# Kernel optimization log

Measured on AMD Instinct MI355X. Metric: run time of the kernel, lower is better.

## Reference

```python
import jax, jax.numpy as jnp
import numpy as np

KK = 9  # 3x3 kernel taps
BN_EPS = 1e-5


def setup_inputs() -> dict:
    key = jax.random.key(0)
    ks = jax.random.split(key, 8)
    B, C, H, W = 2, 64, 256, 256
    O = 64
    x = jax.random.normal(ks[0], (B, C, H, W), dtype=jnp.float32)
    # offset/mask conv: 3*KK output channels (dy[9], dx[9], mask[9])
    w_off = jax.random.normal(ks[1], (3 * KK, C, 3, 3), dtype=jnp.float32) * 0.05
    b_off = jnp.zeros((3 * KK,), dtype=jnp.float32)
    # deformable conv weight
    w = jax.random.normal(ks[2], (O, C, 3, 3), dtype=jnp.float32) * (1.0 / np.sqrt(C * KK))
    b = jnp.zeros((O,), dtype=jnp.float32)
    gamma = jnp.ones((O,), dtype=jnp.float32)
    beta = jnp.zeros((O,), dtype=jnp.float32)
    return {"x": x, "w_off": w_off, "b_off": b_off, "w": w, "b": b,
            "gamma": gamma, "beta": beta}


def _dcn_bn_act_res(x, w_off, b_off, w, b, gamma, beta):
    B, C, H, W = x.shape
    O = w.shape[0]
    # offset/mask prediction via plain 3x3 conv
    om = jax.lax.conv_general_dilated(
        x, w_off, window_strides=(1, 1), padding=[(1, 1), (1, 1)],
        dimension_numbers=("NCHW", "OIHW", "NCHW")) + b_off[None, :, None, None]
    off_y = om[:, :KK]            # [B,9,H,W]
    off_x = om[:, KK:2 * KK]      # [B,9,H,W]
    mask = jax.nn.sigmoid(om[:, 2 * KK:])  # [B,9,H,W] modulation

    # absolute sampling coordinates: base grid + kernel tap offset (-1..1) + learned offset
    ky, kx = jnp.meshgrid(jnp.arange(3), jnp.arange(3), indexing="ij")
    ky = ky.reshape(KK).astype(jnp.float32) - 1.0
    kx = kx.reshape(KK).astype(jnp.float32) - 1.0
    hs = jnp.arange(H, dtype=jnp.float32)
    ws = jnp.arange(W, dtype=jnp.float32)
    py = off_y + hs[None, None, :, None] + ky[None, :, None, None]  # [B,9,H,W]
    px = off_x + ws[None, None, None, :] + kx[None, :, None, None]

    y0 = jnp.floor(py)
    x0 = jnp.floor(px)
    wy = py - y0
    wx = px - x0
    y0i = y0.astype(jnp.int32)
    x0i = x0.astype(jnp.int32)

    def gather(img, yi, xi):
        # img [C,H,W], yi/xi [9,H,W]; zero outside (implicit zero padding)
        valid = (yi >= 0) & (yi < H) & (xi >= 0) & (xi < W)
        yc = jnp.clip(yi, 0, H - 1)
        xc = jnp.clip(xi, 0, W - 1)
        return img[:, yc, xc] * valid[None].astype(img.dtype)  # [C,9,H,W]

    def sample_one(img, yi, xi, wy_, wx_):
        v00 = gather(img, yi, xi)
        v01 = gather(img, yi, xi + 1)
        v10 = gather(img, yi + 1, xi)
        v11 = gather(img, yi + 1, xi + 1)
        w00 = ((1 - wy_) * (1 - wx_))[None]
        w01 = ((1 - wy_) * wx_)[None]
        w10 = (wy_ * (1 - wx_))[None]
        w11 = (wy_ * wx_)[None]
        return v00 * w00 + v01 * w01 + v10 * w10 + v11 * w11  # [C,9,H,W]

    sampled = jax.vmap(sample_one)(x, y0i, x0i, wy, wx)  # [B,C,9,H,W]
    sampled = sampled * mask[:, None]

    out = jnp.einsum("bckhw,ock->bohw", sampled, w.reshape(O, C, KK))
    out = out + b[None, :, None, None]

    # BatchNorm (training-mode batch statistics)
    mu = out.mean(axis=(0, 2, 3), keepdims=True)
    var = out.var(axis=(0, 2, 3), keepdims=True)
    out = (out - mu) * jax.lax.rsqrt(var + BN_EPS)
    out = out * gamma[None, :, None, None] + beta[None, :, None, None]

    return jax.nn.relu(out) + x  # residual


def reference(x, w_off, b_off, w, b, gamma, beta):
    return _dcn_bn_act_res(x, w_off, b_off, w, b, gamma, beta)
```

## Files before the change

kernel.cpp:

```cpp
#include <hip/hip_runtime.h>
#include <hip/hip_fp16.h>
#include <math.h>

#define HWSZ 65536
#define IMGH 256
#define IMGW 256

typedef _Float16 half8 __attribute__((ext_vector_type(8)));
typedef float f32x4 __attribute__((ext_vector_type(4)));

__device__ inline unsigned short f2bf(float f) {
    unsigned u = __float_as_uint(f);
    return (unsigned short)((u + 0x7fffu + ((u >> 16) & 1u)) >> 16);
}
__device__ inline unsigned short f2h(float f) {
    __half h = __float2half(f);
    return __half_as_ushort(h);
}
__device__ inline __half2 duph2(unsigned s) {
    union { unsigned u; __half2 h; } c;
    c.u = (s & 0xffffu) * 0x10001u;
    return c.h;
}
__device__ inline void hacc(const uint4& q, __half2 w, __half2* v) {
    const __half2* h = (const __half2*)&q;
    v[0] = __hfma2(h[0], w, v[0]);
    v[1] = __hfma2(h[1], w, v[1]);
    v[2] = __hfma2(h[2], w, v[2]);
    v[3] = __hfma2(h[3], w, v[3]);
}

__global__ void prep_weights(const float* __restrict__ w_off,
                             const float* __restrict__ w,
                             unsigned short* __restrict__ wApack,
                             unsigned short* __restrict__ wOffPack) {
    int i = blockIdx.x * 256 + threadIdx.x;
    if (i < 36864) {
        int e = i;
        int j = e & 7, lane = (e >> 3) & 63, kk = (e >> 9) & 1;
        int t2 = e >> 10;
        int tap = t2 % 9, g = t2 / 9;
        int o = g * 16 + (lane & 15);
        int c = kk * 32 + ((lane >> 4) & 3) * 8 + j;
        wApack[e] = f2h(w[(o * 64 + c) * 9 + tap]);
    } else if (i < 36864 + 18432) {
        int e = i - 36864;
        int j = e & 7, lane = (e >> 3) & 63, kk = (e >> 9) & 1;
        int t2 = e >> 10;
        int tap = t2 % 9, mt = t2 / 9;
        int d = mt * 16 + (lane & 15);
        int c = kk * 32 + ((lane >> 4) & 3) * 8 + j;
        float v = (d < 27) ? w_off[(d * 64 + c) * 9 + tap] : 0.f;
        wOffPack[e] = f2h(v);
    }
}

__global__ __launch_bounds__(256) void transpose_x(const float* __restrict__ x,
                                                   unsigned short* __restrict__ xT) {
    __shared__ float tile[64 * 65];
    int blk = blockIdx.x;
    int b = blk >> 10;
    int p0 = (blk & 1023) * 64;
    int t = threadIdx.x;
    const float* xb = x + (size_t)b * 64 * HWSZ;
    unsigned short* xTb = xT + (size_t)b * HWSZ * 64;
    int pp = t & 63;
    int c0r = t >> 6;
#pragma unroll
    for (int i = 0; i < 16; ++i) {
        int c = c0r + 4 * i;
        tile[c * 65 + pp] = xb[(size_t)c * HWSZ + p0 + pp];
    }
    __syncthreads();
#pragma unroll
    for (int it = 0; it < 2; ++it) {
        int item = t + it * 256;
        int p = item >> 3;
        int c0 = (item & 7) * 8;
        uint4 ow;
        ow.x = f2h(tile[(c0 + 0) * 65 + p]) | ((unsigned)f2h(tile[(c0 + 1) * 65 + p]) << 16);
        ow.y = f2h(tile[(c0 + 2) * 65 + p]) | ((unsigned)f2h(tile[(c0 + 3) * 65 + p]) << 16);
        ow.z = f2h(tile[(c0 + 4) * 65 + p]) | ((unsigned)f2h(tile[(c0 + 5) * 65 + p]) << 16);
        ow.w = f2h(tile[(c0 + 6) * 65 + p]) | ((unsigned)f2h(tile[(c0 + 7) * 65 + p]) << 16);
        *(uint4*)&xTb[(size_t)(p0 + p) * 64 + c0] = ow;
    }
}

__global__ __launch_bounds__(512, 4) void dcn_main(const unsigned short* __restrict__ xT,
                                                   const unsigned short* __restrict__ wApack,
                                                   const unsigned short* __restrict__ wOffPack,
                                                   const float* __restrict__ b_off,
                                                   unsigned short* __restrict__ preout,
                                                   float* __restrict__ stats) {
    __shared__ uint4 haloBuf[3744];
    __shared__ float om_s[27 * 128];
    __shared__ float bstats[128];
    char* halo = (char*)haloBuf;
    int bid = blockIdx.x;
    int blk = ((bid & 7) << 7) | (bid >> 3);
    int b = blk >> 9;
    int tb = blk & 511;
    int ty = tb >> 5, tx = tb & 31;
    int h0 = ty * 16, w0 = tx * 8;
    int t = threadIdx.x;
    const char* xbb = (const char*)(xT + (size_t)b * HWSZ * 64);
    int lane = t & 63;
    int wid = t >> 6;
    int lp = lane & 15;
    int lhi = lane >> 4;
    unsigned lhi16 = (unsigned)(lhi << 4);
    int p = wid * 16 + lp;
    int hb = h0 - 5, wb = w0 - 5;

    if (t < 128) bstats[t] = 0.f;

    for (int i = t; i < 3744; i += 512) {
        int cell = i >> 3;
        int ch = i & 7;
        int r = cell / 18, c = cell - r * 18;
        int y = hb + r, xx = wb + c;
        uint4 v = {0u, 0u, 0u, 0u};
        if ((unsigned)y < 256u && (unsigned)xx < 256u)
            v = *(const uint4*)(xbb + ((size_t)((y << 8) + xx) << 7) + (ch << 4));
        *(uint4*)(halo + (cell << 7) + ((ch ^ (cell & 7)) << 4)) = v;
    }
    __syncthreads();

    {
        int mt = wid & 1;
        const half8* wp = (const half8*)wOffPack;
        f32x4 z0 = {0.f, 0.f, 0.f, 0.f};
#pragma unroll
        for (int hf = 0; hf < 2; ++hf) {
            int nt = (wid >> 1) + hf * 4;
            int pp = nt * 16 + lp;
            int pr = pp >> 3, pc = pp & 7;
            f32x4 oa = z0;
#pragma unroll
            for (int tap = 0; tap < 9; ++tap) {
                int dy = tap / 3, dx = tap - dy * 3;
                int cell = (pr + dy + 4) * 18 + (pc + dx + 4);
                unsigned ad = (((unsigned)cell << 7) | (((unsigned)cell & 7) << 4)) ^ lhi16;
                half8 b0 = *(const half8*)(halo + ad);
                half8 b1 = *(const half8*)(halo + (ad ^ 64u));
                half8 wa0 = wp[((mt * 9 + tap) * 2 + 0) * 64 + lane];
                half8 wa1 = wp[((mt * 9 + tap) * 2 + 1) * 64 + lane];
                oa = __builtin_amdgcn_mfma_f32_16x16x32_f16(wa0, b0, oa, 0, 0, 0);
                oa = __builtin_amdgcn_mfma_f32_16x16x32_f16(wa1, b1, oa, 0, 0, 0);
            }
#pragma unroll
            for (int jj = 0; jj < 4; ++jj) {
                int d = mt * 16 + lhi * 4 + jj;
                if (d < 27) om_s[d * 128 + pp] = oa[jj] + b_off[d];
            }
        }
    }
    __syncthreads();

    unsigned enc[9];
    uint2 wwr[9];
    {
        int h = h0 + (p >> 3), wc = w0 + (p & 7);
#pragma unroll
        for (int tap = 0; tap < 9; ++tap) {
            float offy = om_s[tap * 128 + p];
            float offx = om_s[(tap + 9) * 128 + p];
            float mraw = om_s[(tap + 18) * 128 + p];
            float m = 1.f / (1.f + __expf(-mraw));
            float pyf = (float)(h + tap / 3 - 1) + offy;
            float pxf = (float)(wc + tap % 3 - 1) + offx;
            float y0f = floorf(pyf), x0f = floorf(pxf);
            float wy = pyf - y0f, wx = pxf - x0f;
            int y0 = (int)y0f, x0 = (int)x0f;
            int y1 = y0 + 1, x1 = x0 + 1;
            float vy0 = (y0 >= 0 && y0 < IMGH) ? 1.f : 0.f;
            float vy1 = (y1 >= 0 && y1 < IMGH) ? 1.f : 0.f;
            float vx0 = (x0 >= 0 && x0 < IMGW) ? 1.f : 0.f;
            float vx1 = (x1 >= 0 && x1 < IMGW) ? 1.f : 0.f;
            float w00 = (1.f - wy) * (1.f - wx) * m * vy0 * vx0;
            float w01 = (1.f - wy) * wx * m * vy0 * vx1;
            float w10 = wy * (1.f - wx) * m * vy1 * vx0;
            float w11 = wy * wx * m * vy1 * vx1;
            wwr[tap] = make_uint2((unsigned)f2h(w00) | ((unsigned)f2h(w01) << 16),
                                  (unsigned)f2h(w10) | ((unsigned)f2h(w11) << 16));
            int ry0 = y0 - hb, rx0 = x0 - wb;
            if ((unsigned)ry0 <= 24u && (unsigned)rx0 <= 16u) {
                enc[tap] = (unsigned)(ry0 * 18 + rx0) << 1;
            } else {
                int y0s = min(max(y0, -8), 383) + 8;
                int x0s = min(max(x0, -8), 383) + 8;
                enc[tap] = 1u | ((unsigned)y0s << 1) | ((unsigned)x0s << 10);
            }
        }
    }

    f32x4 z = {0.f, 0.f, 0.f, 0.f};
    f32x4 acc[4] = {z, z, z, z};
    const half8* ap = (const half8*)wApack;
    uint4 q[4][2];

#define SBASE(CC) ((((CC) << 7) | (((CC) & 7u) << 4)) ^ lhi16)
#define LOADC(E)                                                              \
    {                                                                         \
        unsigned e_ = (E);                                                    \
        bool fb_ = (e_ & 1u);                                                 \
        unsigned cl_ = fb_ ? 0u : (e_ >> 1);                                  \
        unsigned a00 = SBASE(cl_), a01 = SBASE(cl_ + 1u);                     \
        unsigned a10 = SBASE(cl_ + 18u), a11 = SBASE(cl_ + 19u);              \
        q[0][0] = *(const uint4*)(halo + a00);                                \
        q[0][1] = *(const uint4*)(halo + (a00 ^ 64u));                        \
        q[1][0] = *(const uint4*)(halo + a01);                                \
        q[1][1] = *(const uint4*)(halo + (a01 ^ 64u));                        \
        q[2][0] = *(const uint4*)(halo + a10);                                \
        q[2][1] = *(const uint4*)(halo + (a10 ^ 64u));                        \
        q[3][0] = *(const uint4*)(halo + a11);                                \
        q[3][1] = *(const uint4*)(halo + (a11 ^ 64u));                        \
        if (__ballot(fb_)) {                                                  \
            if (fb_) {                                                        \
                int y0r = (int)((e_ >> 1) & 511) - 8;                         \
                int x0r = (int)((e_ >> 10) & 511) - 8;                        \
                int y0c = min(max(y0r, 0), 255), y1c = min(max(y0r + 1, 0), 255); \
                int x0c = min(max(x0r, 0), 255), x1c = min(max(x0r + 1, 0), 255); \
                const char* g00 = xbb + (((y0c << 8) + x0c) << 7) + (lhi << 4); \
                const char* g01 = xbb + (((y0c << 8) + x1c) << 7) + (lhi << 4); \
                const char* g10 = xbb + (((y1c << 8) + x0c) << 7) + (lhi << 4); \
                const char* g11 = xbb + (((y1c << 8) + x1c) << 7) + (lhi << 4); \
                q[0][0] = *(const uint4*)g00; q[0][1] = *(const uint4*)(g00 + 64); \
                q[1][0] = *(const uint4*)g01; q[1][1] = *(const uint4*)(g01 + 64); \
                q[2][0] = *(const uint4*)g10; q[2][1] = *(const uint4*)(g10 + 64); \
                q[3][0] = *(const uint4*)g11; q[3][1] = *(const uint4*)(g11 + 64); \
            }                                                                 \
        }                                                                     \
    }

    LOADC(enc[0]);

#pragma unroll
    for (int tap = 0; tap < 9; ++tap) {
        uint2 ww = wwr[tap];
        __half2 W00 = duph2(ww.x), W01 = duph2(ww.x >> 16);
        __half2 W10 = duph2(ww.y), W11 = duph2(ww.y >> 16);
        union HV { __half2 h2[4]; half8 h8; } V0, V1;
        __half2 z2 = __float2half2_rn(0.f);
#pragma unroll
        for (int j = 0; j < 4; ++j) { V0.h2[j] = z2; V1.h2[j] = z2; }
        hacc(q[0][0], W00, V0.h2); hacc(q[0][1], W00, V1.h2);
        hacc(q[1][0], W01, V0.h2); hacc(q[1][1], W01, V1.h2);
        hacc(q[2][0], W10, V0.h2); hacc(q[2][1], W10, V1.h2);
        hacc(q[3][0], W11, V0.h2); hacc(q[3][1], W11, V1.h2);
        half8 b0 = V0.h8, b1 = V1.h8;
        if (tap < 8) LOADC(enc[tap + 1]);
        __builtin_amdgcn_s_setprio(1);
#pragma unroll
        for (int g2 = 0; g2 < 4; ++g2) {
            half8 a0 = ap[((g2 * 9 + tap) * 2 + 0) * 64 + lane];
            half8 a1 = ap[((g2 * 9 + tap) * 2 + 1) * 64 + lane];
            acc[g2] = __builtin_amdgcn_mfma_f32_16x16x32_f16(a0, b0, acc[g2], 0, 0, 0);
            acc[g2] = __builtin_amdgcn_mfma_f32_16x16x32_f16(a1, b1, acc[g2], 0, 0, 0);
        }
        __builtin_amdgcn_s_setprio(0);
    }
#undef LOADC
#undef SBASE

    unsigned short* pob = preout + (size_t)b * 64 * HWSZ;
    int gp = (h0 + (p >> 3)) * IMGW + w0 + (p & 7);
#pragma unroll
    for (int g2 = 0; g2 < 4; ++g2) {
#pragma unroll
        for (int jj = 0; jj < 4; ++jj) {
            int o = g2 * 16 + lhi * 4 + jj;
            pob[(size_t)o * HWSZ + gp] = f2bf(acc[g2][jj]);
        }
    }
#pragma unroll
    for (int g2 = 0; g2 < 4; ++g2) {
#pragma unroll
        for (int jj = 0; jj < 4; ++jj) {
            float s1 = acc[g2][jj];
            float s2 = s1 * s1;
#pragma unroll
            for (int mask = 1; mask < 16; mask <<= 1) {
                s1 += __shfl_xor(s1, mask);
                s2 += __shfl_xor(s2, mask);
            }
            if (lp == 0) {
                int o = g2 * 16 + lhi * 4 + jj;
                atomicAdd(&bstats[o], s1);
                atomicAdd(&bstats[64 + o], s2);
            }
        }
    }
    __syncthreads();
    if (t < 128) atomicAdd(&stats[t], bstats[t]);
}

__global__ __launch_bounds__(256) void bn_finalize(const float* __restrict__ stats,
                                                   const float* __restrict__ gamma,
                                                   const float* __restrict__ beta,
                                                   const float* __restrict__ x,
                                                   const unsigned short* __restrict__ preout,
                                                   float* __restrict__ out) {
    int i = blockIdx.x * 256 + threadIdx.x;
    int e0 = i * 8;
    int o = (e0 >> 16) & 63;
    const float inv_n = 1.f / 131072.f;
    float mean = stats[o] * inv_n;
    float var = stats[64 + o] * inv_n - mean * mean;
    float rstd = rsqrtf(var + 1e-5f);
    float g = gamma[o] * rstd;
    float bb = beta[o] - mean * g;
    uint4 q = ((const uint4*)preout)[i];
    float4 x0 = ((const float4*)x)[i * 2];
    float4 x1 = ((const float4*)x)[i * 2 + 1];
    float4 r0, r1;
    r0.x = fmaxf(__uint_as_float(q.x << 16) * g + bb, 0.f) + x0.x;
    r0.y = fmaxf(__uint_as_float(q.x & 0xffff0000u) * g + bb, 0.f) + x0.y;
    r0.z = fmaxf(__uint_as_float(q.y << 16) * g + bb, 0.f) + x0.z;
    r0.w = fmaxf(__uint_as_float(q.y & 0xffff0000u) * g + bb, 0.f) + x0.w;
    r1.x = fmaxf(__uint_as_float(q.z << 16) * g + bb, 0.f) + x1.x;
    r1.y = fmaxf(__uint_as_float(q.z & 0xffff0000u) * g + bb, 0.f) + x1.y;
    r1.z = fmaxf(__uint_as_float(q.w << 16) * g + bb, 0.f) + x1.z;
    r1.w = fmaxf(__uint_as_float(q.w & 0xffff0000u) * g + bb, 0.f) + x1.w;
    ((float4*)out)[i * 2] = r0;
    ((float4*)out)[i * 2 + 1] = r1;
}

extern "C" void kernel_launch(void* const* d_in, const int* in_sizes, int n_in,
                              void* d_out, int out_size, void* d_ws, size_t ws_size,
                              hipStream_t stream) {
    const float* x     = (const float*)d_in[0];
    const float* w_off = (const float*)d_in[1];
    const float* b_off = (const float*)d_in[2];
    const float* w     = (const float*)d_in[3];
    const float* gamma = (const float*)d_in[5];
    const float* beta  = (const float*)d_in[6];
    float* out = (float*)d_out;
    char* wsb = (char*)d_ws;

    unsigned short* xT       = (unsigned short*)wsb;
    unsigned short* preout   = (unsigned short*)(wsb + 16777216);
    unsigned short* wApack   = (unsigned short*)(wsb + 33554432);
    unsigned short* wOffPack = (unsigned short*)(wsb + 33628160);
    float*          stats    = (float*)(wsb + 33665024);

    hipMemsetAsync(stats, 0, 512, stream);
    prep_weights<<<216, 256, 0, stream>>>(w_off, w, wApack, wOffPack);
    transpose_x<<<2048, 256, 0, stream>>>(x, xT);
    dcn_main<<<1024, 512, 0, stream>>>(xT, wApack, wOffPack, b_off, preout, stats);
    bn_finalize<<<4096, 256, 0, stream>>>(stats, gamma, beta, x, preout, out);
}
```

Baseline: 104.1 us.

## Distribute bilinear sampling parameter computation across all threads via shared memory

Previously each thread computed sampling encodings and bilinear weights for all 9 taps of its own pixel, even though the 4 lane groups (lhi) sharing a pixel did the same work redundantly. Now the 1152 (tap,pixel) pairs are spread across the 512 threads, written into the reused om_s shared buffer, and read back per tap inside the main loop. This cuts redundant transcendental and ALU work and frees the enc/wwr register arrays. In exchange it adds extra barriers and an LDS read per tap on the critical path.

```diff
diff --git a/kernel.cpp b/kernel.cpp
--- a/kernel.cpp
+++ b/kernel.cpp
@@ -96,6 +96,8 @@
     __shared__ float om_s[27 * 128];
     __shared__ float bstats[128];
     char* halo = (char*)haloBuf;
+    unsigned* prmi = (unsigned*)om_s;
+    uint2* prmw_s = (uint2*)(om_s + 1152);
     int bid = blockIdx.x;
     int blk = ((bid & 7) << 7) | (bid >> 3);
     int b = blk >> 9;
@@ -157,42 +159,53 @@
     }
     __syncthreads();
 
-    unsigned enc[9];
-    uint2 wwr[9];
+#define PARAMS(I, EOUT, WOUT)                                                 \
+    {                                                                         \
+        int i_ = (I);                                                         \
+        int tp_ = i_ >> 7, pp_ = i_ & 127;                                    \
+        int hh_ = h0 + (pp_ >> 3), wc_ = w0 + (pp_ & 7);                      \
+        float offy = om_s[tp_ * 128 + pp_];                                   \
+        float offx = om_s[(tp_ + 9) * 128 + pp_];                             \
+        float mraw = om_s[(tp_ + 18) * 128 + pp_];                            \
+        float m_ = 1.f / (1.f + __expf(-mraw));                               \
+        float pyf = (float)(hh_ + tp_ / 3 - 1) + offy;                        \
+        float pxf = (float)(wc_ + tp_ % 3 - 1) + offx;                        \
+        float y0f = floorf(pyf), x0f = floorf(pxf);                           \
+        float wy = pyf - y0f, wx = pxf - x0f;                                 \
+        int y0_ = (int)y0f, x0_ = (int)x0f;                                   \
+        int y1_ = y0_ + 1, x1_ = x0_ + 1;                                     \
+        float vy0 = (y0_ >= 0 && y0_ < IMGH) ? 1.f : 0.f;                     \
+        float vy1 = (y1_ >= 0 && y1_ < IMGH) ? 1.f : 0.f;                     \
+        float vx0 = (x0_ >= 0 && x0_ < IMGW) ? 1.f : 0.f;                     \
+        float vx1 = (x1_ >= 0 && x1_ < IMGW) ? 1.f : 0.f;                     \
+        float w00 = (1.f - wy) * (1.f - wx) * m_ * vy0 * vx0;                 \
+        float w01 = (1.f - wy) * wx * m_ * vy0 * vx1;                         \
+        float w10 = wy * (1.f - wx) * m_ * vy1 * vx0;                         \
+        float w11 = wy * wx * m_ * vy1 * vx1;                                 \
+        WOUT = make_uint2((unsigned)f2h(w00) | ((unsigned)f2h(w01) << 16),    \
+                          (unsigned)f2h(w10) | ((unsigned)f2h(w11) << 16));   \
+        int ry0 = y0_ - hb, rx0 = x0_ - wb;                                   \
+        if ((unsigned)ry0 <= 24u && (unsigned)rx0 <= 16u) {                   \
+            EOUT = (unsigned)(ry0 * 18 + rx0) << 1;                           \
+        } else {                                                              \
+            int y0s = min(max(y0_, -8), 383) + 8;                             \
+            int x0s = min(max(x0_, -8), 383) + 8;                             \
+            EOUT = 1u | ((unsigned)y0s << 1) | ((unsigned)x0s << 10);         \
+        }                                                                     \
+    }
     {
-        int h = h0 + (p >> 3), wc = w0 + (p & 7);
-#pragma unroll
-        for (int tap = 0; tap < 9; ++tap) {
-            float offy = om_s[tap * 128 + p];
-            float offx = om_s[(tap + 9) * 128 + p];
-            float mraw = om_s[(tap + 18) * 128 + p];
-            float m = 1.f / (1.f + __expf(-mraw));
-            float pyf = (float)(h + tap / 3 - 1) + offy;
-            float pxf = (float)(wc + tap % 3 - 1) + offx;
-            float y0f = floorf(pyf), x0f = floorf(pxf);
-            float wy = pyf - y0f, wx = pxf - x0f;
-            int y0 = (int)y0f, x0 = (int)x0f;
-            int y1 = y0 + 1, x1 = x0 + 1;
-            float vy0 = (y0 >= 0 && y0 < IMGH) ? 1.f : 0.f;
-            float vy1 = (y1 >= 0 && y1 < IMGH) ? 1.f : 0.f;
-            float vx0 = (x0 >= 0 && x0 < IMGW) ? 1.f : 0.f;
-            float vx1 = (x1 >= 0 && x1 < IMGW) ? 1.f : 0.f;
-            float w00 = (1.f - wy) * (1.f - wx) * m * vy0 * vx0;
-            float w01 = (1.f - wy) * wx * m * vy0 * vx1;
-            float w10 = wy * (1.f - wx) * m * vy1 * vx0;
-            float w11 = wy * wx * m * vy1 * vx1;
-            wwr[tap] = make_uint2((unsigned)f2h(w00) | ((unsigned)f2h(w01) << 16),
-                                  (unsigned)f2h(w10) | ((unsigned)f2h(w11) << 16));
-            int ry0 = y0 - hb, rx0 = x0 - wb;
-            if ((unsigned)ry0 <= 24u && (unsigned)rx0 <= 16u) {
-                enc[tap] = (unsigned)(ry0 * 18 + rx0) << 1;
-            } else {
-                int y0s = min(max(y0, -8), 383) + 8;
-                int x0s = min(max(x0, -8), 383) + 8;
-                enc[tap] = 1u | ((unsigned)y0s << 1) | ((unsigned)x0s << 10);
-            }
-        }
-    }
+        unsigned pe0, pe1, pe2 = 0;
+        uint2 pw0 = make_uint2(0, 0), pw1 = pw0, pw2 = pw0;
+        PARAMS(t, pe0, pw0);
+        PARAMS(t + 512, pe1, pw1);
+        if (t < 128) PARAMS(t + 1024, pe2, pw2);
+        __syncthreads();
+        prmi[t] = pe0;        prmw_s[t] = pw0;
+        prmi[t + 512] = pe1;  prmw_s[t + 512] = pw1;
+        if (t < 128) { prmi[t + 1024] = pe2; prmw_s[t + 1024] = pw2; }
+    }
+#undef PARAMS
+    __syncthreads();
 
     f32x4 z = {0.f, 0.f, 0.f, 0.f};
     f32x4 acc[4] = {z, z, z, z};
@@ -233,11 +246,12 @@
         }                                                                     \
     }
 
-    LOADC(enc[0]);
+    unsigned pi = prmi[p];
+    uint2 ww = prmw_s[p];
+    LOADC(pi);
 
 #pragma unroll
     for (int tap = 0; tap < 9; ++tap) {
-        uint2 ww = wwr[tap];
         __half2 W00 = duph2(ww.x), W01 = duph2(ww.x >> 16);
         __half2 W10 = duph2(ww.y), W11 = duph2(ww.y >> 16);
         union HV { __half2 h2[4]; half8 h8; } V0, V1;
@@ -249,7 +263,11 @@
         hacc(q[2][0], W10, V0.h2); hacc(q[2][1], W10, V1.h2);
         hacc(q[3][0], W11, V0.h2); hacc(q[3][1], W11, V1.h2);
         half8 b0 = V0.h8, b1 = V1.h8;
-        if (tap < 8) LOADC(enc[tap + 1]);
+        if (tap < 8) {
+            pi = prmi[(tap + 1) * 128 + p];
+            ww = prmw_s[(tap + 1) * 128 + p];
+            LOADC(pi);
+        }
         __builtin_amdgcn_s_setprio(1);
 #pragma unroll
         for (int g2 = 0; g2 < 4; ++g2) {
```

New measurement: 93.88 us. -9.8%, faster.
